# Performance work log

Hardware: AMD Instinct MI355X
Metric: run time of the kernel (lower is better)

Reference implementation:

```python
import jax, jax.numpy as jnp
import numpy as np

EPS = 1e-6


def layernorm(x, w, b):
    m = jnp.mean(x, axis=-1, keepdims=True)
    v = jnp.var(x, axis=-1, keepdims=True)
    return (x - m) * jax.lax.rsqrt(v + EPS) * w + b


def rotate_half(x):
    x1, x2 = jnp.split(x, 2, axis=-1)
    return jnp.concatenate((-x2, x1), axis=-1)


def setup_inputs() -> dict:
    key = jax.random.key(0)
    ks = jax.random.split(key, 16)
    T, D, H, HD, I = 16384, 1280, 16, 80, 5120
    NSEG = 16
    inp = {
        "hidden_states": jax.random.normal(ks[0], (T, D), jnp.float32),
        "cos": jax.random.uniform(ks[1], (T, HD), jnp.float32),
        "sin": jax.random.uniform(ks[2], (T, HD), jnp.float32),
        "ln1_w": jnp.ones((D,), jnp.float32),
        "ln1_b": jnp.zeros((D,), jnp.float32),
        "ln2_w": jnp.ones((D,), jnp.float32),
        "ln2_b": jnp.zeros((D,), jnp.float32),
        "qkv_w": jax.random.normal(ks[3], (3 * D, D), jnp.float32) * 0.02,
        "qkv_b": jnp.zeros((3 * D,), jnp.float32),
        "proj_w": jax.random.normal(ks[4], (D, D), jnp.float32) * 0.02,
        "proj_b": jnp.zeros((D,), jnp.float32),
        "fc1_w": jax.random.normal(ks[5], (I, D), jnp.float32) * 0.02,
        "fc1_b": jnp.zeros((I,), jnp.float32),
        "fc2_w": jax.random.normal(ks[6], (D, I), jnp.float32) * 0.02,
        "fc2_b": jnp.zeros((D,), jnp.float32),
        "cu_seqlens": jnp.arange(NSEG + 1, dtype=jnp.int32) * (T // NSEG),
    }
    return inp


def reference(hidden_states, cos, sin, ln1_w, ln1_b, ln2_w, ln2_b,
              qkv_w, qkv_b, proj_w, proj_b, fc1_w, fc1_b, fc2_w, fc2_b,
              cu_seqlens):
    T, D = hidden_states.shape
    H = 16
    HD = D // H
    nseg = cu_seqlens.shape[0] - 1  # equal-length segments by construction
    L = T // nseg

    x = layernorm(hidden_states, ln1_w, ln1_b)
    qkv = (x @ qkv_w.T + qkv_b).reshape(T, 3, H, HD)
    q, k, v = qkv[:, 0], qkv[:, 1], qkv[:, 2]  # [T, H, HD]

    # RoPE in fp32, cos/sin broadcast over heads
    c = cos[:, None, :]
    s = sin[:, None, :]
    q = q * c + rotate_half(q) * s
    k = k * c + rotate_half(k) * s

    # block-diagonal varlen attention: reshape into [nseg, L, H, HD]
    qs = q.reshape(nseg, L, H, HD)
    ks = k.reshape(nseg, L, H, HD)
    vs = v.reshape(nseg, L, H, HD)
    scale = 1.0 / jnp.sqrt(jnp.asarray(HD, jnp.float32))
    scores = jnp.einsum('slhd,smhd->shlm', qs, ks) * scale
    probs = jax.nn.softmax(scores, axis=-1)
    attn = jnp.einsum('shlm,smhd->slhd', probs, vs).reshape(T, D)

    attn_out = attn @ proj_w.T + proj_b
    h = hidden_states + attn_out

    y = layernorm(h, ln2_w, ln2_b)
    mlp = (jax.nn.silu(y @ fc1_w.T + fc1_b)) @ fc2_w.T + fc2_b
    return h + mlp
```

## Files before the change

### kernel.cpp

```cpp
#include <hip/hip_runtime.h>
#include <hip/hip_bf16.h>
#include <hip/hip_fp16.h>

typedef _Float16 f16;
typedef _Float16 f16x4 __attribute__((ext_vector_type(4)));
typedef _Float16 f16x8 __attribute__((ext_vector_type(8)));
typedef float f32x4 __attribute__((ext_vector_type(4)));

#define T_TOK 16384
#define D_MOD 1280
#define N_QKV 3840
#define I_MLP 5120
#define N_HEAD 16
#define HD 80
#define SEG_L 1024

__device__ __forceinline__ void async16(const void* g, void* l) {
    __builtin_amdgcn_global_load_lds(
        (const __attribute__((address_space(1))) void*)g,
        (__attribute__((address_space(3))) void*)l, 16, 0, 0);
}

#define BAR()        asm volatile("s_barrier" ::: "memory")
#define WAIT_LGKM0() do { asm volatile("s_waitcnt lgkmcnt(0)" ::: "memory"); \
                          __builtin_amdgcn_sched_barrier(0); } while (0)
#define WAIT_VM(n)   asm volatile("s_waitcnt vmcnt(" #n ")" ::: "memory")

__global__ __launch_bounds__(256) void cast_f32_f16(
    const float* __restrict__ src, f16* __restrict__ dst, int n) {
    int i = blockIdx.x * 256 + threadIdx.x;
    if (i < n) dst[i] = (f16)src[i];
}

template <typename TIN>
__global__ __launch_bounds__(256) void ln_kernel(
    const TIN* __restrict__ x, const float* __restrict__ w,
    const float* __restrict__ b, f16* __restrict__ out) {
    const int t = blockIdx.x;
    const TIN* row = x + (size_t)t * D_MOD;
    float vals[5];
    float s = 0.f, s2 = 0.f;
    for (int i = 0; i < 5; ++i) {
        float v = (float)row[threadIdx.x + i * 256];
        vals[i] = v; s += v; s2 += v * v;
    }
    for (int off = 32; off > 0; off >>= 1) {
        s  += __shfl_down(s, off);
        s2 += __shfl_down(s2, off);
    }
    __shared__ float rs[4], rs2[4];
    int wv = threadIdx.x >> 6;
    if ((threadIdx.x & 63) == 0) { rs[wv] = s; rs2[wv] = s2; }
    __syncthreads();
    s  = rs[0] + rs[1] + rs[2] + rs[3];
    s2 = rs2[0] + rs2[1] + rs2[2] + rs2[3];
    float m = s * (1.f / D_MOD);
    float var = s2 * (1.f / D_MOD) - m * m;
    float rstd = rsqrtf(var + 1e-6f);
    for (int i = 0; i < 5; ++i) {
        int c = threadIdx.x + i * 256;
        out[(size_t)t * D_MOD + c] = (f16)((vals[i] - m) * rstd * w[c] + b[c]);
    }
}

__global__ __launch_bounds__(256) void rope_inplace(
    f16* __restrict__ q, f16* __restrict__ k,
    const float* __restrict__ cosb, const float* __restrict__ sinb) {
    int i = blockIdx.x * 256 + threadIdx.x;
    if (i >= T_TOK * N_HEAD * 40) return;
    int d = i % 40;
    int th = i / 40;
    int h = th & 15;
    int t = th >> 4;
    size_t i0 = ((size_t)h * T_TOK + t) * HD + d;
    size_t i1 = i0 + 40;
    float c0 = cosb[t * HD + d],      s0 = sinb[t * HD + d];
    float c1 = cosb[t * HD + d + 40], s1 = sinb[t * HD + d + 40];
    {
        float x0 = (float)q[i0], x1 = (float)q[i1];
        q[i0] = (f16)(x0 * c0 - x1 * s0);
        q[i1] = (f16)(x1 * c1 + x0 * s1);
    }
    {
        float x0 = (float)k[i0], x1 = (float)k[i1];
        k[i0] = (f16)(x0 * c0 - x1 * s0);
        k[i1] = (f16)(x1 * c1 + x0 * s1);
    }
}

#define EPI_QKV   0
#define EPI_PROJ  1
#define EPI_SILU  2
#define EPI_FC2A  3
#define EPI_FC2B  4

#define READ_A(MH) \
    _Pragma("unroll") for (int mi = 0; mi < 4; ++mi) { \
        const f16* pa = &LB[lb][MH][(wr * 64 + mi * 16 + lane16) * 64]; \
        aF[mi][0] = *(const f16x8*)&pa[ch0]; \
        aF[mi][1] = *(const f16x8*)&pa[ch1]; \
    }
#define READ_B(NH) \
    _Pragma("unroll") for (int ni = 0; ni < 2; ++ni) { \
        const f16* pb = &LB[lb][2 + NH][(wc * 32 + ni * 16 + lane16) * 64]; \
        bF[ni][0] = *(const f16x8*)&pb[ch0]; \
        bF[ni][1] = *(const f16x8*)&pb[ch1]; \
    }
#define DO_MFMA(MH, NH) \
    __builtin_amdgcn_s_setprio(1); \
    _Pragma("unroll") for (int mi = 0; mi < 4; ++mi) \
    _Pragma("unroll") for (int ni = 0; ni < 2; ++ni) { \
        acc[MH][NH][mi][ni] = __builtin_amdgcn_mfma_f32_16x16x32_f16( \
            aF[mi][0], bF[ni][0], acc[MH][NH][mi][ni], 0, 0, 0); \
        acc[MH][NH][mi][ni] = __builtin_amdgcn_mfma_f32_16x16x32_f16( \
            aF[mi][1], bF[ni][1], acc[MH][NH][mi][ni], 0, 0, 0); \
    } \
    __builtin_amdgcn_s_setprio(0);

template <int EPI>
__global__ __launch_bounds__(512, 2) void gemm_bt(
    const f16* __restrict__ A, const f16* __restrict__ B,
    const float* __restrict__ bias, const void* __restrict__ resid,
    void* __restrict__ out0, f16* __restrict__ out1, f16* __restrict__ out2,
    int M, int N, int K, int lda, int ldb, int ldo) {
    __shared__ __align__(16) f16 LB[2][4][8192];
    const int tid = threadIdx.x;
    const int w = tid >> 6;
    const int l = tid & 63;
    const int lane16 = l & 15, quad = l >> 4;
    const int wr = w >> 2, wc = w & 3;

    const int nx = gridDim.x;
    int id = blockIdx.y * nx + blockIdx.x;
    const int nwg = nx * gridDim.y;
    int tile = ((nwg & 7) == 0) ? ((id & 7) * (nwg >> 3) + (id >> 3)) : id;
    const int m0 = (tile / nx) * 256;
    const int n0 = (tile % nx) * 256;
    const int NT = K >> 6;

    const int rr = tid >> 3;
    const int cc = (tid & 7) ^ (rr & 7);
    const size_t ga_off = (size_t)rr * lda + cc * 8;
    const size_t gb_off = (size_t)rr * ldb + cc * 8;
    const int lds_off = w * 512;
    const int swz = lane16 & 7;
    const int ch0 = ((0 * 4 + quad) ^ swz) * 8;
    const int ch1 = ((1 * 4 + quad) ^ swz) * 8;

    f32x4 acc[2][2][4][2];
#pragma unroll
    for (int a = 0; a < 2; ++a)
#pragma unroll
        for (int b2 = 0; b2 < 2; ++b2)
#pragma unroll
            for (int c = 0; c < 4; ++c)
#pragma unroll
                for (int d = 0; d < 2; ++d)
                    acc[a][b2][c][d] = (f32x4){0.f, 0.f, 0.f, 0.f};

    const f16* Abase = A + (size_t)m0 * lda;
    const f16* Bbase = B + (size_t)n0 * ldb;
    auto stageA = [&](int buf, int ph, int t) {
        const f16* g = Abase + (size_t)(ph * 128) * lda + (size_t)t * 64 + ga_off;
        f16* lr = &LB[buf][ph][0] + lds_off;
        async16(g, lr);
        async16(g + (size_t)64 * lda, lr + 4096);
    };
    auto stageB = [&](int buf, int ph, int t) {
        const f16* g = Bbase + (size_t)(ph * 128) * ldb + (size_t)t * 64 + gb_off;
        f16* lr = &LB[buf][2 + ph][0] + lds_off;
        async16(g, lr);
        async16(g + (size_t)64 * ldb, lr + 4096);
    };

    stageA(0, 0, 0); stageB(0, 1, 0); stageA(0, 1, 0); stageB(0, 0, 0);
    if (NT > 1) {
        stageA(1, 0, 1); stageB(1, 1, 1); stageA(1, 1, 1);
        WAIT_VM(6);
    } else {
        WAIT_VM(0);
    }
    BAR();

    for (int t = 0; t < NT; ++t) {
        const int lb = t & 1;
        f16x8 aF[4][2], bF[2][2];
        READ_A(0); READ_B(0);
        { int tau = t + 1; if (tau < NT) stageB(tau & 1, 0, tau); }
        BAR(); WAIT_LGKM0();
        DO_MFMA(0, 0);
        BAR();
        READ_B(1);
        { int tau = t + 2; if (tau < NT) stageA(tau & 1, 0, tau); }
        BAR(); WAIT_LGKM0();
        DO_MFMA(0, 1);
        BAR();
        READ_A(1);
        { int tau = t + 2; if (tau < NT) stageB(tau & 1, 1, tau); }
        BAR(); WAIT_LGKM0();
        DO_MFMA(1, 1);
        BAR();
        READ_B(0);
        { int tau = t + 2; if (tau < NT) stageA(tau & 1, 1, tau); }
        BAR(); WAIT_LGKM0();
        DO_MFMA(1, 0);
        if (t < NT - 2) { WAIT_VM(6); } else { WAIT_VM(0); }
        BAR();
    }

#pragma unroll
    for (int mh = 0; mh < 2; ++mh)
#pragma unroll
    for (int mi = 0; mi < 4; ++mi) {
        const int row = m0 + mh * 128 + wr * 64 + mi * 16 + quad * 4;
#pragma unroll
        for (int nh = 0; nh < 2; ++nh)
#pragma unroll
        for (int ni = 0; ni < 2; ++ni) {
            const int col = n0 + nh * 128 + wc * 32 + ni * 16 + lane16;
            const f32x4 v4 = acc[mh][nh][mi][ni];
            float bv = (EPI == EPI_FC2B) ? 0.f : bias[col];
            if (EPI == EPI_QKV) {
                int g = col / D_MOD;
                int rem = col - g * D_MOD;
                int h = rem / HD, d = rem - h * HD;
                if (g == 2) {
                    f16x4 pk;
#pragma unroll
                    for (int r2 = 0; r2 < 4; ++r2) pk[r2] = (f16)(v4[r2] + bv);
                    f16* dst = out2 + ((size_t)h * HD + d) * T_TOK + row;
                    *(f16x4*)dst = pk;
                } else {
                    f16* dst = (g == 0) ? (f16*)out0 : out1;
                    size_t base = ((size_t)h * T_TOK) * HD + d;
#pragma unroll
                    for (int r2 = 0; r2 < 4; ++r2) {
                        float v = v4[r2] + bv;
                        dst[base + (size_t)(row + r2) * HD] = (f16)v;
                    }
                }
            } else {
#pragma unroll
                for (int r2 = 0; r2 < 4; ++r2) {
                    float v = v4[r2] + bv;
                    size_t idx = (size_t)(row + r2) * ldo + col;
                    if (EPI == EPI_PROJ) {
                        ((f16*)out0)[idx] = (f16)(v + ((const float*)resid)[idx]);
                    } else if (EPI == EPI_SILU) {
                        ((f16*)out0)[idx] = (f16)(v / (1.f + __expf(-v)));
                    } else if (EPI == EPI_FC2A) {
                        ((float*)out0)[idx] = v + (float)((const f16*)resid)[idx];
                    } else {
                        ((float*)out0)[idx] += v;
                    }
                }
            }
        }
    }
}

#undef READ_A
#undef READ_B
#undef DO_MFMA

#define QK_STRIDE 104
#define VT_STRIDE 72
#define P_STRIDE  72
__global__ __launch_bounds__(256, 3) void attn_kernel(
    const f16* __restrict__ q, const f16* __restrict__ k,
    const f16* __restrict__ vt, f16* __restrict__ out) {
    const int bid = blockIdx.x;
    const int s = bid >> 8, h = (bid >> 4) & 15, qt = bid & 15;
    const int t0 = s * SEG_L;
    __shared__ f16 lQ[64 * QK_STRIDE];
    __shared__ f16 lK[64 * QK_STRIDE];
    __shared__ f16 lVt[80 * VT_STRIDE];
    __shared__ f16 lP[4 * 16 * P_STRIDE];
    const int tid = threadIdx.x;
    const int w = tid >> 6, l = tid & 63;
    const int lane16 = l & 15, quad = l >> 4;
    const f16 scale = (f16)0.16132167f;

    const f16* qbase  = q  + (size_t)h * T_TOK * HD + (size_t)(t0 + qt * 64) * HD;
    const f16* kbase  = k  + (size_t)h * T_TOK * HD + (size_t)t0 * HD;
    const f16* vtbase = vt + (size_t)h * HD * T_TOK + t0;

    for (int idx = tid; idx < 64 * 12; idx += 256) {
        int r = idx / 12, c8 = idx % 12;
        f16x8 val = (f16x8){0, 0, 0, 0, 0, 0, 0, 0};
        if (c8 < 10) {
            val = *(const f16x8*)&qbase[r * 80 + c8 * 8];
            val = val * scale;
        }
        *(f16x8*)&lQ[r * QK_STRIDE + c8 * 8] = val;
    }
    for (int idx = tid; idx < 64 * 2; idx += 256) {
        int r = idx >> 1, c8 = 10 + (idx & 1);
        *(f16x8*)&lK[r * QK_STRIDE + c8 * 8] = (f16x8){0, 0, 0, 0, 0, 0, 0, 0};
    }

    float lrow[4] = {0.f, 0.f, 0.f, 0.f};
    f32x4 o[5];
    for (int i = 0; i < 5; ++i) o[i] = (f32x4){0.f, 0.f, 0.f, 0.f};

    for (int kt = 0; kt < 16; ++kt) {
        __syncthreads();
        for (int idx = tid; idx < 64 * 10; idx += 256) {
            int r = idx / 10, c8 = idx % 10;
            *(f16x8*)&lK[r * QK_STRIDE + c8 * 8] =
                *(const f16x8*)&kbase[(kt * 64 + r) * 80 + c8 * 8];
        }
        for (int idx = tid; idx < 80 * 8; idx += 256) {
            int d = idx / 8, r8 = idx % 8;
            *(f16x8*)&lVt[d * VT_STRIDE + r8 * 8] =
                *(const f16x8*)&vtbase[(size_t)d * T_TOK + kt * 64 + r8 * 8];
        }
        __syncthreads();

        f32x4 sacc[4];
        for (int ct = 0; ct < 4; ++ct) {
            f32x4 a = (f32x4){0.f, 0.f, 0.f, 0.f};
            for (int ks = 0; ks < 3; ++ks) {
                f16x8 af = *(const f16x8*)&lQ[(w * 16 + lane16) * QK_STRIDE + ks * 32 + quad * 8];
                f16x8 bf = *(const f16x8*)&lK[(ct * 16 + lane16) * QK_STRIDE + ks * 32 + quad * 8];
                a = __builtin_amdgcn_mfma_f32_16x16x32_f16(af, bf, a, 0, 0, 0);
            }
            sacc[ct] = a;
        }

        for (int ct = 0; ct < 4; ++ct) {
            for (int r = 0; r < 4; ++r) {
                float p = __builtin_exp2f(fminf(sacc[ct][r], 14.f));
                lrow[r] += p;
                lP[w * 16 * P_STRIDE + (quad * 4 + r) * P_STRIDE + ct * 16 + lane16] = (f16)p;
            }
        }

        for (int vt2 = 0; vt2 < 5; ++vt2) {
            for (int ks = 0; ks < 2; ++ks) {
                f16x8 af = *(const f16x8*)&lP[w * 16 * P_STRIDE + lane16 * P_STRIDE + ks * 32 + quad * 8];
                f16x8 bf = *(const f16x8*)&lVt[(vt2 * 16 + lane16) * VT_STRIDE + ks * 32 + quad * 8];
                o[vt2] = __builtin_amdgcn_mfma_f32_16x16x32_f16(af, bf, o[vt2], 0, 0, 0);
            }
        }
    }

    for (int r = 0; r < 4; ++r)
        for (int off = 1; off < 16; off <<= 1)
            lrow[r] += __shfl_xor(lrow[r], off);

    f16* obase = out + (size_t)(t0 + qt * 64 + w * 16) * D_MOD + h * HD;
    for (int r = 0; r < 4; ++r) {
        float inv = 1.f / lrow[r];
        for (int vt2 = 0; vt2 < 5; ++vt2) {
            int row = quad * 4 + r;
            int hd = vt2 * 16 + lane16;
            obase[(size_t)row * D_MOD + hd] = (f16)(o[vt2][r] * inv);
        }
    }
}

extern "C" void kernel_launch(void* const* d_in, const int* in_sizes, int n_in,
                              void* d_out, int out_size, void* d_ws, size_t ws_size,
                              hipStream_t stream) {
    const float* hidden = (const float*)d_in[0];
    const float* cosb   = (const float*)d_in[1];
    const float* sinb   = (const float*)d_in[2];
    const float* ln1w   = (const float*)d_in[3];
    const float* ln1b   = (const float*)d_in[4];
    const float* ln2w   = (const float*)d_in[5];
    const float* ln2b   = (const float*)d_in[6];
    const float* qkvw   = (const float*)d_in[7];
    const float* qkvb   = (const float*)d_in[8];
    const float* projw  = (const float*)d_in[9];
    const float* projb  = (const float*)d_in[10];
    const float* fc1w   = (const float*)d_in[11];
    const float* fc1b   = (const float*)d_in[12];
    const float* fc2w   = (const float*)d_in[13];
    const float* fc2b   = (const float*)d_in[14];
    float* out = (float*)d_out;

    f16* wqkv  = (f16*)d_ws;
    f16* wproj = wqkv  + 4915200;
    f16* wfc1  = wproj + 1638400;
    f16* wfc2  = wfc1  + 6553600;
    f16* qf    = wfc2  + 6553600;
    f16* kf    = qf    + 20971520;
    f16* vf    = kf    + 20971520;
    f16* xf    = vf    + 20971520;
    f16* hbuf  = xf    + 20971520;
    f16* attnf  = xf;
    f16* yf     = qf;
    f16* fc1out = kf;

    cast_f32_f16<<<(4915200 + 255) / 256, 256, 0, stream>>>(qkvw, wqkv, 4915200);
    cast_f32_f16<<<(1638400 + 255) / 256, 256, 0, stream>>>(projw, wproj, 1638400);
    cast_f32_f16<<<(6553600 + 255) / 256, 256, 0, stream>>>(fc1w, wfc1, 6553600);
    cast_f32_f16<<<(6553600 + 255) / 256, 256, 0, stream>>>(fc2w, wfc2, 6553600);

    ln_kernel<float><<<T_TOK, 256, 0, stream>>>(hidden, ln1w, ln1b, xf);

    gemm_bt<EPI_QKV><<<dim3(N_QKV / 256, T_TOK / 256), 512, 0, stream>>>(
        xf, wqkv, qkvb, nullptr, qf, kf, vf,
        T_TOK, N_QKV, D_MOD, D_MOD, D_MOD, 0);

    rope_inplace<<<(T_TOK * N_HEAD * 40) / 256, 256, 0, stream>>>(qf, kf, cosb, sinb);

    attn_kernel<<<16 * 16 * 16, 256, 0, stream>>>(qf, kf, vf, attnf);

    gemm_bt<EPI_PROJ><<<dim3(D_MOD / 256, T_TOK / 256), 512, 0, stream>>>(
        attnf, wproj, projb, hidden, hbuf, nullptr, nullptr,
        T_TOK, D_MOD, D_MOD, D_MOD, D_MOD, D_MOD);

    ln_kernel<f16><<<T_TOK, 256, 0, stream>>>(hbuf, ln2w, ln2b, yf);

    for (int c = 0; c < 2; ++c) {
        gemm_bt<EPI_SILU><<<dim3(2560 / 256, T_TOK / 256), 512, 0, stream>>>(
            yf, wfc1 + (size_t)c * 2560 * D_MOD, fc1b + c * 2560, nullptr,
            fc1out, nullptr, nullptr,
            T_TOK, 2560, D_MOD, D_MOD, D_MOD, 2560);
        if (c == 0) {
            gemm_bt<EPI_FC2A><<<dim3(D_MOD / 256, T_TOK / 256), 512, 0, stream>>>(
                fc1out, wfc2, fc2b, hbuf, out, nullptr, nullptr,
                T_TOK, D_MOD, 2560, 2560, I_MLP, D_MOD);
        } else {
            gemm_bt<EPI_FC2B><<<dim3(D_MOD / 256, T_TOK / 256), 512, 0, stream>>>(
                fc1out, wfc2 + 2560, fc2b, nullptr, out, nullptr, nullptr,
                T_TOK, D_MOD, 2560, 2560, I_MLP, D_MOD);
        }
    }
}
```

Measured before the change: 1.509 ms.

## Restructure attention with 32x32 MFMA, register Q/P, swizzled LDS and prefetch

Rewrites the attention kernel so each block handles 128 query rows, with each wave owning 32 rows. Q fragments stay in registers, and S^T is computed with 32x32x16 MFMAs so probabilities pass to the PV MFMA through lane shuffles instead of an LDS round trip. K/V tiles use XOR-swizzled LDS to avoid bank conflicts and are prefetched into registers one tile ahead, overlapping global loads with compute. The grid is remapped for locality and occupancy drops to 2 blocks per SM; the changes aim to cut LDS traffic and K/V reloads, at the cost of more register pressure.

```diff
diff --git a/kernel.cpp b/kernel.cpp
--- a/kernel.cpp
+++ b/kernel.cpp
@@ -3,9 +3,12 @@
 #include <hip/hip_fp16.h>
 
 typedef _Float16 f16;
+typedef _Float16 f16x2 __attribute__((ext_vector_type(2)));
 typedef _Float16 f16x4 __attribute__((ext_vector_type(4)));
 typedef _Float16 f16x8 __attribute__((ext_vector_type(8)));
 typedef float f32x4 __attribute__((ext_vector_type(4)));
+typedef float f32x16 __attribute__((ext_vector_type(16)));
+typedef int i32x4 __attribute__((ext_vector_type(4)));
 
 #define T_TOK 16384
 #define D_MOD 1280
@@ -25,6 +28,9 @@
 #define WAIT_LGKM0() do { asm volatile("s_waitcnt lgkmcnt(0)" ::: "memory"); \
                           __builtin_amdgcn_sched_barrier(0); } while (0)
 #define WAIT_VM(n)   asm volatile("s_waitcnt vmcnt(" #n ")" ::: "memory")
+
+__device__ __forceinline__ int f2i(f16x2 v) { int r; __builtin_memcpy(&r, &v, 4); return r; }
+__device__ __forceinline__ f16x2 i2f(int v) { f16x2 r; __builtin_memcpy(&r, &v, 4); return r; }
 
 __global__ __launch_bounds__(256) void cast_f32_f16(
     const float* __restrict__ src, f16* __restrict__ dst, int n) {
@@ -263,99 +269,147 @@
 #undef READ_B
 #undef DO_MFMA
 
-#define QK_STRIDE 104
-#define VT_STRIDE 72
-#define P_STRIDE  72
-__global__ __launch_bounds__(256, 3) void attn_kernel(
+__global__ __launch_bounds__(256, 2) void attn_kernel(
     const f16* __restrict__ q, const f16* __restrict__ k,
     const f16* __restrict__ vt, f16* __restrict__ out) {
-    const int bid = blockIdx.x;
-    const int s = bid >> 8, h = (bid >> 4) & 15, qt = bid & 15;
+    const int bid0 = blockIdx.x;
+    const int bid = (bid0 & 7) * 256 + (bid0 >> 3);
+    const int s = bid >> 7, h = (bid >> 3) & 15, qt = bid & 7;
     const int t0 = s * SEG_L;
-    __shared__ f16 lQ[64 * QK_STRIDE];
-    __shared__ f16 lK[64 * QK_STRIDE];
-    __shared__ f16 lVt[80 * VT_STRIDE];
-    __shared__ f16 lP[4 * 16 * P_STRIDE];
     const int tid = threadIdx.x;
     const int w = tid >> 6, l = tid & 63;
-    const int lane16 = l & 15, quad = l >> 4;
+    const int l31 = l & 31, hi = l >> 5;
+
+    __shared__ __align__(16) f16 lK[64 * 128];
+    __shared__ __align__(16) f16 lVt[96 * 64];
+    __shared__ float lInv[128];
+
     const f16 scale = (f16)0.16132167f;
 
-    const f16* qbase  = q  + (size_t)h * T_TOK * HD + (size_t)(t0 + qt * 64) * HD;
+    const int qrow_g = t0 + qt * 128 + w * 32 + l31;
+    const f16* qp = q + ((size_t)h * T_TOK + qrow_g) * HD;
+    f16x8 qf[5];
+#pragma unroll
+    for (int ks = 0; ks < 5; ++ks) {
+        f16x8 v = *(const f16x8*)&qp[(ks * 2 + hi) * 8];
+        qf[ks] = v * scale;
+    }
+
     const f16* kbase  = k  + (size_t)h * T_TOK * HD + (size_t)t0 * HD;
     const f16* vtbase = vt + (size_t)h * HD * T_TOK + t0;
 
-    for (int idx = tid; idx < 64 * 12; idx += 256) {
-        int r = idx / 12, c8 = idx % 12;
-        f16x8 val = (f16x8){0, 0, 0, 0, 0, 0, 0, 0};
-        if (c8 < 10) {
-            val = *(const f16x8*)&qbase[r * 80 + c8 * 8];
-            val = val * scale;
-        }
-        *(f16x8*)&lQ[r * QK_STRIDE + c8 * 8] = val;
-    }
-    for (int idx = tid; idx < 64 * 2; idx += 256) {
-        int r = idx >> 1, c8 = 10 + (idx & 1);
-        *(f16x8*)&lK[r * QK_STRIDE + c8 * 8] = (f16x8){0, 0, 0, 0, 0, 0, 0, 0};
-    }
-
-    float lrow[4] = {0.f, 0.f, 0.f, 0.f};
-    f32x4 o[5];
-    for (int i = 0; i < 5; ++i) o[i] = (f32x4){0.f, 0.f, 0.f, 0.f};
+    if (tid < 128) {
+        int r = 80 + (tid >> 3), c = tid & 7;
+        *(f16x8*)&lVt[r * 64 + ((c ^ (r & 7)) * 8)] = (f16x8){0,0,0,0,0,0,0,0};
+    }
+
+    f16x8 kreg[3], vreg[3];
+    auto ld_tile = [&](int kt) {
+#pragma unroll
+        for (int j = 0; j < 3; ++j) {
+            int idx = tid + j * 256;
+            if (idx < 640) {
+                int r = idx / 10, c = idx - r * 10;
+                kreg[j] = *(const f16x8*)&kbase[(size_t)(kt * 64 + r) * HD + c * 8];
+                int rv = idx >> 3, cv = idx & 7;
+                vreg[j] = *(const f16x8*)&vtbase[(size_t)rv * T_TOK + kt * 64 + cv * 8];
+            }
+        }
+    };
+    auto st_tile = [&]() {
+#pragma unroll
+        for (int j = 0; j < 3; ++j) {
+            int idx = tid + j * 256;
+            if (idx < 640) {
+                int r = idx / 10, c = idx - r * 10;
+                *(f16x8*)&lK[r * 128 + ((c ^ (r & 7)) * 8)] = kreg[j];
+                int rv = idx >> 3, cv = idx & 7;
+                *(f16x8*)&lVt[rv * 64 + ((cv ^ (rv & 7)) * 8)] = vreg[j];
+            }
+        }
+    };
+
+    float lrow = 0.f;
+    f32x16 zz;
+#pragma unroll
+    for (int i = 0; i < 16; ++i) zz[i] = 0.f;
+    f32x16 oacc[3];
+    oacc[0] = zz; oacc[1] = zz; oacc[2] = zz;
+
+    ld_tile(0);
+    st_tile();
+    __syncthreads();
 
     for (int kt = 0; kt < 16; ++kt) {
+        if (kt < 15) ld_tile(kt + 1);
+
+#pragma unroll
+        for (int ct = 0; ct < 2; ++ct) {
+            f32x16 sc = zz;
+#pragma unroll
+            for (int ks = 0; ks < 5; ++ks) {
+                const int row = ct * 32 + l31;
+                f16x8 kf = *(const f16x8*)&lK[row * 128 +
+                              (((ks * 2 + hi) ^ (l31 & 7)) * 8)];
+                sc = __builtin_amdgcn_mfma_f32_32x32x16_f16(kf, qf[ks], sc, 0, 0, 0);
+            }
+            float pf[16];
+#pragma unroll
+            for (int r = 0; r < 16; ++r) {
+                float p = __builtin_exp2f(fminf(sc[r], 14.f));
+                lrow += p;
+                pf[r] = p;
+            }
+            f16x2 own[4][2];
+            int prt[4][2];
+#pragma unroll
+            for (int d = 0; d < 4; ++d) {
+                own[d][0] = (f16x2){(f16)pf[4 * d + 0], (f16)pf[4 * d + 1]};
+                own[d][1] = (f16x2){(f16)pf[4 * d + 2], (f16)pf[4 * d + 3]};
+                prt[d][0] = __shfl_xor(f2i(own[d][0]), 32);
+                prt[d][1] = __shfl_xor(f2i(own[d][1]), 32);
+            }
+#pragma unroll
+            for (int kk2 = 0; kk2 < 2; ++kk2) {
+                const int De = 2 * kk2, Do = 2 * kk2 + 1;
+                i32x4 av;
+                av[0] = hi ? prt[Do][0] : f2i(own[De][0]);
+                av[1] = hi ? prt[Do][1] : f2i(own[De][1]);
+                av[2] = hi ? f2i(own[Do][0]) : prt[De][0];
+                av[3] = hi ? f2i(own[Do][1]) : prt[De][1];
+                f16x8 af;
+                __builtin_memcpy(&af, &av, 16);
+                const int kkg = ct * 2 + kk2;
+#pragma unroll
+                for (int nt = 0; nt < 3; ++nt) {
+                    const int vrow = nt * 32 + l31;
+                    f16x8 vf = *(const f16x8*)&lVt[vrow * 64 +
+                                  (((kkg * 2 + hi) ^ (l31 & 7)) * 8)];
+                    oacc[nt] = __builtin_amdgcn_mfma_f32_32x32x16_f16(
+                        af, vf, oacc[nt], 0, 0, 0);
+                }
+            }
+        }
         __syncthreads();
-        for (int idx = tid; idx < 64 * 10; idx += 256) {
-            int r = idx / 10, c8 = idx % 10;
-            *(f16x8*)&lK[r * QK_STRIDE + c8 * 8] =
-                *(const f16x8*)&kbase[(kt * 64 + r) * 80 + c8 * 8];
-        }
-        for (int idx = tid; idx < 80 * 8; idx += 256) {
-            int d = idx / 8, r8 = idx % 8;
-            *(f16x8*)&lVt[d * VT_STRIDE + r8 * 8] =
-                *(const f16x8*)&vtbase[(size_t)d * T_TOK + kt * 64 + r8 * 8];
-        }
+        if (kt < 15) st_tile();
         __syncthreads();
-
-        f32x4 sacc[4];
-        for (int ct = 0; ct < 4; ++ct) {
-            f32x4 a = (f32x4){0.f, 0.f, 0.f, 0.f};
-            for (int ks = 0; ks < 3; ++ks) {
-                f16x8 af = *(const f16x8*)&lQ[(w * 16 + lane16) * QK_STRIDE + ks * 32 + quad * 8];
-                f16x8 bf = *(const f16x8*)&lK[(ct * 16 + lane16) * QK_STRIDE + ks * 32 + quad * 8];
-                a = __builtin_amdgcn_mfma_f32_16x16x32_f16(af, bf, a, 0, 0, 0);
-            }
-            sacc[ct] = a;
-        }
-
-        for (int ct = 0; ct < 4; ++ct) {
-            for (int r = 0; r < 4; ++r) {
-                float p = __builtin_exp2f(fminf(sacc[ct][r], 14.f));
-                lrow[r] += p;
-                lP[w * 16 * P_STRIDE + (quad * 4 + r) * P_STRIDE + ct * 16 + lane16] = (f16)p;
-            }
-        }
-
-        for (int vt2 = 0; vt2 < 5; ++vt2) {
-            for (int ks = 0; ks < 2; ++ks) {
-                f16x8 af = *(const f16x8*)&lP[w * 16 * P_STRIDE + lane16 * P_STRIDE + ks * 32 + quad * 8];
-                f16x8 bf = *(const f16x8*)&lVt[(vt2 * 16 + lane16) * VT_STRIDE + ks * 32 + quad * 8];
-                o[vt2] = __builtin_amdgcn_mfma_f32_16x16x32_f16(af, bf, o[vt2], 0, 0, 0);
-            }
-        }
-    }
-
-    for (int r = 0; r < 4; ++r)
-        for (int off = 1; off < 16; off <<= 1)
-            lrow[r] += __shfl_xor(lrow[r], off);
-
-    f16* obase = out + (size_t)(t0 + qt * 64 + w * 16) * D_MOD + h * HD;
-    for (int r = 0; r < 4; ++r) {
-        float inv = 1.f / lrow[r];
-        for (int vt2 = 0; vt2 < 5; ++vt2) {
-            int row = quad * 4 + r;
-            int hd = vt2 * 16 + lane16;
-            obase[(size_t)row * D_MOD + hd] = (f16)(o[vt2][r] * inv);
+    }
+
+    lrow += __shfl_xor(lrow, 32);
+    float inv = 1.f / lrow;
+    lInv[w * 32 + l31] = inv;
+
+    f16* obase = out + (size_t)(t0 + qt * 128 + w * 32) * D_MOD + h * HD;
+#pragma unroll
+    for (int nt = 0; nt < 3; ++nt) {
+        const int hd = nt * 32 + l31;
+        if (nt < 2 || l31 < 16) {
+#pragma unroll
+            for (int r = 0; r < 16; ++r) {
+                const int qrow = (r & 3) + 8 * (r >> 2) + 4 * hi;
+                obase[(size_t)qrow * D_MOD + hd] =
+                    (f16)(oacc[nt][r] * lInv[w * 32 + qrow]);
+            }
         }
     }
 }
@@ -406,7 +460,7 @@
 
     rope_inplace<<<(T_TOK * N_HEAD * 40) / 256, 256, 0, stream>>>(qf, kf, cosb, sinb);
 
-    attn_kernel<<<16 * 16 * 16, 256, 0, stream>>>(qf, kf, vf, attnf);
+    attn_kernel<<<2048, 256, 0, stream>>>(qf, kf, vf, attnf);
 
     gemm_bt<EPI_PROJ><<<dim3(D_MOD / 256, T_TOK / 256), 512, 0, stream>>>(
         attnf, wproj, projb, hidden, hbuf, nullptr, nullptr,
```

After: 1.393 ms. 7.7% less time.
